# Kernel tuning notes

Measured on AMD Instinct MI355X. Metric: run time of the kernel, lower is better.

Reference implementation:

```python
import jax, jax.numpy as jnp
import numpy as np

B, T, C, D = 4, 2048, 48, 512
L = 16                    # transcript length per video (distinct labels)
K = 9                     # bdy_kernel
CS = 15                   # cs_kernel
N_TR = L - 1
N_CAND = 3 * N_TR         # candidate_mul * pt_num
WIN_LEN = int(T / L * 0.15)   # int(t / t_len * win_scale)
ALPHA, BETA, GAMMA, TEMP = 1.0, 1.0, 0.1, 0.1
LOG2 = float(np.log(2.0))

def _bdy_kernel():
    ker = np.zeros((K, K), np.float32)
    c = K // 2
    ker[:c, :c] = 1; ker[c:, c:] = 1
    ker[:c, c:] = -1; ker[c:, :c] = -1
    ker[c, c] = 0
    return jnp.asarray(ker)

BDY_KER = _bdy_kernel()

def bdy_score_fn(prob):
    # prob: [T, C]; sliding windows of size K over time (zero padded)
    c = K // 2
    pad = jnp.pad(prob, ((c, c), (0, 0)))
    win = pad[jnp.arange(T)[:, None] + jnp.arange(K)[None, :]]       # [T,K,C]
    p = win[:, :, None, :]                                           # [T,K,1,C]
    m = (p + win[:, None, :, :]) / 2                                 # [T,K,K,C]
    # torch F.kl_div((m+1e-32).log(), p) = p*(log p - log(m+1e-32)), xlogy(0)=0
    kl = jnp.sum(jnp.where(p > 0, p * (jnp.log(jnp.where(p > 0, p, 1.0)) - jnp.log(m + 1e-32)), 0.0), -1)
    js = (kl + jnp.swapaxes(kl, 1, 2)) / 2
    js = -(js / LOG2 * 2 - 1)                                        # [T,K,K]
    return jnp.mean(BDY_KER[None] * js, axis=(-1, -2))               # [T]

def dp(cls_score):
    # cls_score: [N_TR, N_CAND]; min-cost alignment DP, inner jj-loop vectorized
    cost = -cls_score
    n_tr, n_x = N_TR, N_CAND
    W = 2 * n_tr + 1
    col = jnp.arange(W)
    inf = jnp.float32(jnp.inf)
    tr_at = jnp.clip(col // 2, 0, n_tr - 1)
    even = (col % 2 == 0)
    ge2 = col >= 2

    def init_cols(ii):
        c0 = jnp.where(ii < n_x - n_tr, 0.0, inf)
        c1 = jnp.where(ii <= n_x - n_tr, cost[0, ii], inf)
        d1 = jnp.where(ii <= n_x - n_tr, 1, 0).astype(jnp.int32)
        return c0, c1, d1

    c0, c1, d1 = init_cols(0)
    row0 = jnp.full((W,), inf).at[0].set(c0).at[1].set(c1)
    dir0 = jnp.zeros((W,), jnp.int32).at[1].set(d1)

    def step(prev, ii):
        dm1 = jnp.concatenate([jnp.full((1,), inf), prev[:-1]])
        dm2 = jnp.concatenate([jnp.full((2,), inf), prev[:-2]])
        c_at = cost[:, ii][tr_at]
        even_val = jnp.minimum(prev, dm1)
        even_dir = jnp.where(prev < dm1, 0, 1).astype(jnp.int32)
        odd_val = c_at + jnp.minimum(dm1, dm2)
        odd_dir = jnp.where(dm1 < dm2, 1, 2).astype(jnp.int32)
        c0, c1, d1 = init_cols(ii)
        new = jnp.where(ge2, jnp.where(even, even_val, odd_val), inf)
        new = new.at[0].set(c0).at[1].set(c1)
        dirs = jnp.where(ge2, jnp.where(even, even_dir, odd_dir), 0).astype(jnp.int32)
        dirs = dirs.at[1].set(d1)
        return new, dirs

    last, dirs = jax.lax.scan(step, row0, jnp.arange(1, n_x))
    dir_mat = jnp.concatenate([dir0[None], dirs], 0)                 # [n_x, W]
    cur_j0 = jnp.where(last[2 * n_tr] < last[2 * n_tr - 1], 2 * n_tr, 2 * n_tr - 1).astype(jnp.int32)

    def bt(cur_j, x):
        ii, dir_row = x
        is_odd = (cur_j % 2) == 1
        out_idx = jnp.where(is_odd, cur_j // 2, jnp.int32(n_tr))     # n_tr = OOB -> dropped
        new_j = cur_j - dir_row[cur_j]
        return new_j, (out_idx, ii.astype(jnp.int32))

    _, (oi, ovals) = jax.lax.scan(bt, cur_j0, (jnp.arange(n_x), dir_mat), reverse=True)
    return jnp.zeros((n_tr,), jnp.int32).at[oi].set(ovals, mode='drop')

def detect(logit, tr):
    # logit: [T,C] (detached), tr: [L] ints -> boundary frame indices [N_TR]
    prob = jax.nn.softmax(logit, -1)
    score = bdy_score_fn(prob).at[0].set(-jnp.inf)
    backup = score
    pos = jnp.arange(T)

    def pick(s, _):
        i = jnp.argmax(s)
        return jnp.where(jnp.abs(pos - i) <= WIN_LEN, -jnp.inf, s), i

    _, cand = jax.lax.scan(pick, score, None, length=N_CAND)
    cand = jnp.sort(cand)                                            # [N_CAND]
    # class-transition score at candidate points
    cc = CS // 2
    pairs = jnp.pad(prob[:, tr], ((cc, cc), (0, 0)))                 # [T+2cc, L]
    win = pairs[cand[:, None] + jnp.arange(CS)[None, :]]             # [N_CAND, CS, L]
    first, second = win[:, :, :-1], win[:, :, 1:]
    k0 = jnp.where(jnp.arange(CS) < cc, 1.0, -1.0)[None, :, None]
    cls = jnp.sum(k0 * (first - second), axis=1) / (2 * CS)          # [N_CAND, N_TR]
    cls = cls.T + backup[cand][None, :]                              # [N_TR, N_CAND]
    return cand[dp(cls)]

def _forward(tok_logit, fr_logit, vid_multi_hot, feat, mask, transcript):
    y = vid_multi_hot
    tok_loss = jnp.mean(-(y * jax.nn.log_sigmoid(tok_logit) + (1 - y) * jax.nn.log_sigmoid(-tok_logit)))
    # boundary detection on detached logits
    bdy = jax.vmap(detect)(jax.lax.stop_gradient(fr_logit), transcript)   # [B, N_TR]
    pse = jax.vmap(lambda b, tr: tr[jnp.sum(jnp.arange(T)[:, None] >= b[None, :], axis=1)])(bdy, transcript)
    # frame CE (bgw==1.0 path, full mask so no -100 labels)
    logp = jax.nn.log_softmax(fr_logit, -1)
    ce = -jnp.take_along_axis(logp, pse[..., None], axis=-1)[..., 0]
    m = mask.astype(ce.dtype)
    fr_loss = jnp.sum(ce * m) / jnp.sum(m)
    # global-local contrast
    tok_feat = jax.lax.stop_gradient(feat[:, :C, :])
    fr_feat = feat[:, C:, :]

    def glc_one(tok, fr, pse_i, tr, m_i):
        labels = jnp.sort(tr)                                        # = unique(pse[mask]), distinct labels
        oh = (pse_i[None, :] == labels[:, None]).astype(fr.dtype) * m_i[None, :]
        cnt = jnp.maximum(jnp.sum(oh, 1, keepdims=True), 1.0)
        la = (oh @ fr) / cnt
        la = la / jnp.maximum(jnp.linalg.norm(la, axis=-1, keepdims=True), 1e-12)
        tk = tok / jnp.maximum(jnp.linalg.norm(tok, axis=-1, keepdims=True), 1e-12)
        sim = (la @ tk.T) / TEMP                                     # [L, C]
        return jnp.mean(-jnp.take_along_axis(jax.nn.log_softmax(sim, -1), labels[:, None], axis=-1))

    glc_loss = jnp.mean(jax.vmap(glc_one)(tok_feat, fr_feat, pse, transcript, mask.astype(feat.dtype)))
    return ALPHA * tok_loss + BETA * fr_loss + GAMMA * glc_loss

def setup_inputs() -> dict:
    key = jax.random.key(0)
    ks = jax.random.split(key, 5)
    tok_logit = jax.random.normal(ks[0], (B, C), jnp.float32)
    fr_logit = jax.random.normal(ks[1], (B, T, C), jnp.float32)
    mask = jnp.ones((B, T), bool)
    transcript = jax.vmap(lambda k: jax.random.permutation(k, C)[:L])(jax.random.split(ks[2], B)).astype(jnp.int32)
    vid_multi_hot = jax.random.uniform(ks[3], (B, C), jnp.float32)
    feat = jax.random.normal(ks[4], (B, C + T, D), jnp.float32)
    return {"epoch": 5, "tok_logit": tok_logit, "fr_logit": fr_logit, "mask": mask,
            "transcript": transcript, "vid_multi_hot": vid_multi_hot, "feat": feat}

def reference(epoch, tok_logit, fr_logit, mask, transcript, vid_multi_hot, feat):
    # epoch >= warm_epc (=0), so the full loss path runs
    return _forward(tok_logit, fr_logit, vid_multi_hot, feat, mask, transcript)
```

## Files before the change

### kernel.cpp

```cpp
#include <hip/hip_runtime.h>
#include <math.h>

#define BB 4
#define TT 2048
#define CC 48
#define DD 512
#define LL 16
#define NTR 15
#define NCAND 45
#define WINLEN 19
#define CSW 15
#define CCHALF 7

static __device__ __forceinline__ float wave_reduce_sum(float v) {
    for (int off = 32; off; off >>= 1) v += __shfl_down(v, off);
    return v;
}

#define DPPMAX(x, ctrl) fmaxf((x), __int_as_float(__builtin_amdgcn_update_dpp( \
    __float_as_int(x), __float_as_int(x), (ctrl), 0xF, 0xF, false)))

__global__ __launch_bounds__(256) void k_lse(const float* __restrict__ fr,
                                             float* __restrict__ lse) {
    int row = blockIdx.x * 4 + (threadIdx.x >> 6);
    int lane = threadIdx.x & 63;
    float xv = (lane < CC) ? fr[(size_t)row * CC + lane] : -INFINITY;
    float m = xv;
    for (int off = 32; off; off >>= 1) m = fmaxf(m, __shfl_down(m, off));
    m = __shfl(m, 0);
    float e = (lane < CC) ? __expf(xv - m) : 0.f;
    float s = wave_reduce_sum(e);
    if (lane == 0) lse[row] = m + __logf(s);
}

__global__ __launch_bounds__(256) void k_score(const float* __restrict__ fr,
                                               const float* __restrict__ lse,
                                               float* __restrict__ score) {
    int t_base = (blockIdx.x * 4) % TT;
    int b = (blockIdx.x * 4) / TT;
    __shared__ float sp[12][CC];
    __shared__ float slp[12][CC];
    __shared__ float lse_s[12];
    int tid = threadIdx.x;
    int wave = tid >> 6, lane = tid & 63;
    if (tid < 12) {
        int r = t_base - 4 + tid;
        lse_s[tid] = (r >= 0 && r < TT) ? lse[b * TT + r] : 0.f;
    }
    __syncthreads();
    for (int idx = tid; idx < 12 * CC; idx += 256) {
        int i = idx / CC, c = idx - (idx / CC) * CC;
        int r = t_base - 4 + i;
        float pv = 0.f, lv = 0.f;
        if (r >= 0 && r < TT) {
            float x = fr[((size_t)b * TT + r) * CC + c];
            lv = x - lse_s[i];
            pv = __expf(lv);
        }
        sp[i][c] = pv;
        slp[i][c] = lv;
    }
    __syncthreads();
    int t = t_base + wave;
    float acc = 0.f;
    for (int idx = lane; idx < 4 * CC; idx += 64) {
        int i = idx / CC, c = idx - (idx / CC) * CC;
        acc += -2.f * sp[wave + i][c] * slp[wave + i][c];
    }
    for (int item = lane; item < 36 * CC; item += 64) {
        int pidx = item / CC, c = item - pidx * CC;
        int i = 0, rem = pidx;
        while (rem >= 8 - i) { rem -= 8 - i; ++i; }
        int j = i + 1 + rem;
        float wgt = ((i < 4) == (j < 4)) ? 1.f : -1.f;
        float pi = sp[wave + i][c], pj = sp[wave + j][c];
        float logm = __logf(0.5f * (pi + pj) + 1e-32f);
        acc -= wgt * (pi + pj) * logm;
    }
    acc = wave_reduce_sum(acc);
    if (lane == 0) {
        const float SC = -2.0f / (81.0f * 0.6931471805599453f);
        score[(size_t)b * TT + t] = (t == 0) ? -INFINITY : SC * acc;
    }
}

__global__ __launch_bounds__(64) void k_pick(const float* __restrict__ score,
                                             int* __restrict__ cand,
                                             float* __restrict__ backup) {
    int b = blockIdx.x;
    int lane = threadIdx.x;
    __shared__ float s[64 * 33];
    __shared__ int cl[NCAND];
    for (int t = lane; t < TT; t += 64) s[t + (t >> 5)] = score[(size_t)b * TT + t];
    __syncthreads();
    float v[32];
    #pragma unroll
    for (int k = 0; k < 32; ++k) v[k] = s[lane * 33 + k];
    int base = lane << 5;
    for (int it = 0; it < NCAND; ++it) {
        float best = -INFINITY; int bi = 0;
        #pragma unroll
        for (int k = 31; k >= 0; --k)
            if (v[k] >= best) { best = v[k]; bi = k; }
        float m = best;
        m = DPPMAX(m, 0x111); m = DPPMAX(m, 0x112);
        m = DPPMAX(m, 0x114); m = DPPMAX(m, 0x118);
        m = DPPMAX(m, 0x142); m = DPPMAX(m, 0x143);
        float gmax = __int_as_float(__builtin_amdgcn_readlane(__float_as_int(m), 63));
        unsigned long long ball = __ballot(best == gmax);
        int sl = (int)(__ffsll((long long)ball) - 1);
        int mp = __builtin_amdgcn_readlane(base + bi, sl);
        if (lane == 0) cl[it] = mp;
        int llo = mp - WINLEN - base;
        int lhi = mp + WINLEN - base;
        unsigned lowm = (llo <= 0) ? 0xffffffffu : ((llo >= 32) ? 0u : ~((1u << llo) - 1u));
        unsigned him  = (lhi >= 31) ? 0xffffffffu : ((lhi < 0) ? 0u : ((2u << lhi) - 1u));
        unsigned wm = lowm & him;
        #pragma unroll
        for (int k = 0; k < 32; ++k)
            if (wm & (1u << k)) v[k] = -INFINITY;
    }
    __syncthreads();
    if (lane < NCAND) {
        int my = cl[lane];
        int rank = 0;
        for (int i = 0; i < NCAND; ++i) rank += (cl[i] < my) ? 1 : 0;
        cand[b * 64 + rank] = my;
        backup[b * 64 + rank] = s[my + (my >> 5)];
    }
}

__global__ __launch_bounds__(256) void k_cls(const float* __restrict__ fr,
                                             const float* __restrict__ lse,
                                             const int* __restrict__ cand,
                                             const float* __restrict__ backup,
                                             const int* __restrict__ transcript,
                                             float* __restrict__ cost_g) {
    int ii = blockIdx.x, b = blockIdx.y;
    __shared__ float win[CSW][LL + 1];
    __shared__ int tr_s[LL];
    int tid = threadIdx.x;
    if (tid < LL) tr_s[tid] = transcript[b * LL + tid];
    __syncthreads();
    int cpos = cand[b * 64 + ii];
    if (tid < CSW * LL) {
        int k = tid >> 4, m2 = tid & 15;
        int r = cpos - CCHALF + k;
        float p = 0.f;
        if (r >= 0 && r < TT) {
            size_t ro = (size_t)b * TT + r;
            p = __expf(fr[ro * CC + tr_s[m2]] - lse[ro]);
        }
        win[k][m2] = p;
    }
    __syncthreads();
    if (tid < NTR) {
        int j = tid;
        float sum = 0.f;
        #pragma unroll
        for (int k = 0; k < CSW; ++k)
            sum += ((k < CCHALF) ? 1.f : -1.f) * (win[k][j] - win[k][j + 1]);
        cost_g[(b * NTR + j) * NCAND + ii] = -(sum / 30.f + backup[b * 64 + ii]);
    }
}

__global__ __launch_bounds__(256) void k_dp(const float* __restrict__ fr,
                                            const float* __restrict__ lse,
                                            const int* __restrict__ cand,
                                            const float* __restrict__ cost_g,
                                            const int* __restrict__ transcript,
                                            int* __restrict__ labels_out,
                                            int* __restrict__ rowmap,
                                            float* __restrict__ fr_part,
                                            float* __restrict__ la) {
    int b = blockIdx.x;
    __shared__ float cost[NTR][NCAND];
    __shared__ int tr_s[LL];
    __shared__ int cand_s[NCAND];
    __shared__ signed char dir_mat[NCAND][32];
    __shared__ int bdy_s[NTR];
    __shared__ int rank_s[LL];
    __shared__ float redf[4];
    int tid = threadIdx.x;
    int wave = tid >> 6, lane = tid & 63;
    if (tid < LL) tr_s[tid] = transcript[b * LL + tid];
    if (tid < NCAND) cand_s[tid] = cand[b * 64 + tid];

    {
        float4 z = {0.f, 0.f, 0.f, 0.f};
        float4* lz = (float4*)(la + (size_t)b * LL * DD);
        #pragma unroll
        for (int i = 0; i < LL * DD / 4 / 256; ++i) lz[i * 256 + tid] = z;
    }
    for (int e = tid; e < NTR * NCAND; e += 256) {
        int j = e / NCAND, ii = e - j * NCAND;
        cost[j][ii] = cost_g[b * NTR * NCAND + e];
    }
    __syncthreads();

    if (tid < 64) {
        float prev = INFINITY;
        if (tid == 0) prev = 0.f;
        if (tid == 1) prev = cost[0][0];
        if (tid < 31) dir_mat[0][tid] = (tid == 1) ? (signed char)1 : (signed char)0;
        for (int ii = 1; ii < NCAND; ++ii) {
            float dm1 = __shfl_up(prev, 1); if (tid < 1) dm1 = INFINITY;
            float dm2 = __shfl_up(prev, 2); if (tid < 2) dm2 = INFINITY;
            int trat = tid >> 1; if (trat > NTR - 1) trat = NTR - 1;
            float c_at = cost[trat][ii];
            float ev = fminf(prev, dm1);
            int ed = (prev < dm1) ? 0 : 1;
            float ov = c_at + fminf(dm1, dm2);
            int od = (dm1 < dm2) ? 1 : 2;
            float nv; int nd;
            if (tid >= 2) {
                if ((tid & 1) == 0) { nv = ev; nd = ed; }
                else { nv = ov; nd = od; }
            } else { nv = INFINITY; nd = 0; }
            if (tid == 0) { nv = (ii < NCAND - NTR) ? 0.f : INFINITY; nd = 0; }
            if (tid == 1) {
                nv = (ii <= NCAND - NTR) ? cost[0][ii] : INFINITY;
                nd = (ii <= NCAND - NTR) ? 1 : 0;
            }
            prev = nv;
            if (tid < 31) dir_mat[ii][tid] = (signed char)nd;
        }
        float v29 = __shfl(prev, 29);
        float v30 = __shfl(prev, 30);
        if (tid == 0) {
            int cur = (v30 < v29) ? 30 : 29;
            for (int ii = NCAND - 1; ii >= 0; --ii) {
                if (cur & 1) bdy_s[cur >> 1] = cand_s[ii];
                cur -= (int)dir_mat[ii][cur];
            }
        }
    }
    __syncthreads();

    if (tid < LL) {
        int myv = tr_s[tid];
        int r2 = 0;
        #pragma unroll
        for (int l2 = 0; l2 < LL; ++l2) r2 += (tr_s[l2] < myv) ? 1 : 0;
        rank_s[tid] = r2;
        labels_out[b * LL + r2] = myv;
    }
    __syncthreads();

    float facc = 0.f;
    for (int t = tid; t < TT; t += 256) {
        int cnt = 0;
        #pragma unroll
        for (int j = 0; j < NTR; ++j) cnt += (t >= bdy_s[j]) ? 1 : 0;
        int pv = tr_s[cnt];
        rowmap[b * TT + t] = rank_s[cnt];
        size_t ro = (size_t)b * TT + t;
        facc += lse[ro] - fr[ro * CC + pv];
    }
    facc = wave_reduce_sum(facc);
    if (lane == 0) redf[wave] = facc;
    __syncthreads();
    if (tid == 0) fr_part[b] = redf[0] + redf[1] + redf[2] + redf[3];
}

__global__ __launch_bounds__(256) void k_la(const float* __restrict__ feat,
                                            const int* __restrict__ rowmap,
                                            float* __restrict__ la) {
    int b = blockIdx.y;
    int t0 = blockIdx.x * 32;
    int tid = threadIdx.x;
    const float* frf = feat + ((size_t)b * (CC + TT) + CC) * DD;
    __shared__ int rm[32];
    if (tid < 32) rm[tid] = rowmap[b * TT + t0 + tid];
    __syncthreads();
    float ax = 0.f, ay = 0.f;
    int cur = rm[0];
    for (int k = 0; k < 32; ++k) {
        int r = rm[k];
        if (r != cur) {
            float* dst = la + ((size_t)b * LL + cur) * DD + tid * 2;
            atomicAdd(dst, ax);
            atomicAdd(dst + 1, ay);
            ax = 0.f; ay = 0.f; cur = r;
        }
        const float2* p = (const float2*)(frf + (size_t)(t0 + k) * DD);
        float2 v = p[tid];
        ax += v.x; ay += v.y;
    }
    float* dst = la + ((size_t)b * LL + cur) * DD + tid * 2;
    atomicAdd(dst, ax);
    atomicAdd(dst + 1, ay);
}

__global__ __launch_bounds__(256) void k_glc(const float* __restrict__ feat,
                                             const float* __restrict__ la,
                                             float* __restrict__ dots,
                                             float* __restrict__ ntk) {
    int c = blockIdx.x, b = blockIdx.y;
    __shared__ float tok_s[DD];
    __shared__ float redv[4];
    int tid = threadIdx.x;
    int wave = tid >> 6, lane = tid & 63;
    const float* tr = feat + ((size_t)b * (CC + TT) + c) * DD;
    float2 tv = ((const float2*)tr)[tid];
    ((float2*)tok_s)[tid] = tv;
    float vv = tv.x * tv.x + tv.y * tv.y;
    vv = wave_reduce_sum(vv);
    if (lane == 0) redv[wave] = vv;
    __syncthreads();
    if (tid == 0)
        ntk[b * CC + c] = fmaxf(sqrtf(redv[0] + redv[1] + redv[2] + redv[3]), 1e-12f);
    for (int l = wave; l < LL; l += 4) {
        const float4* lar = (const float4*)(la + ((size_t)b * LL + l) * DD);
        const float4* ts = (const float4*)tok_s;
        float dot = 0.f;
        #pragma unroll
        for (int jj = 0; jj < 2; ++jj) {
            int j = lane + jj * 64;
            float4 a = lar[j]; float4 w = ts[j];
            dot += a.x * w.x + a.y * w.y + a.z * w.z + a.w * w.w;
        }
        dot = wave_reduce_sum(dot);
        if (lane == 0) dots[((size_t)b * LL + l) * CC + c] = dot;
    }
}

__global__ __launch_bounds__(64) void k_term(const float* __restrict__ la,
                                             const float* __restrict__ dots,
                                             const float* __restrict__ ntk,
                                             const int* __restrict__ labels,
                                             float* __restrict__ terms) {
    int l = blockIdx.x, b = blockIdx.y;
    int lane = threadIdx.x;
    const float4* lar = (const float4*)(la + ((size_t)b * LL + l) * DD);
    float ss = 0.f;
    #pragma unroll
    for (int jj = 0; jj < 2; ++jj) {
        float4 a = lar[lane + jj * 64];
        ss += a.x * a.x + a.y * a.y + a.z * a.z + a.w * a.w;
    }
    ss = wave_reduce_sum(ss);
    float nla = fmaxf(sqrtf(__shfl(ss, 0)), 1e-12f);
    float sim = -INFINITY;
    if (lane < CC)
        sim = dots[((size_t)b * LL + l) * CC + lane] * 10.0f / (nla * ntk[b * CC + lane]);
    float mx = sim;
    for (int off = 32; off; off >>= 1) mx = fmaxf(mx, __shfl_down(mx, off));
    mx = __shfl(mx, 0);
    float e = (lane < CC) ? expf(sim - mx) : 0.f;
    float se = wave_reduce_sum(e);
    se = __shfl(se, 0);
    int lab = labels[b * LL + l];
    float sim_lab = __shfl(sim, lab);
    if (lane == 0) terms[b * LL + l] = (mx + logf(se)) - sim_lab;
}

__global__ __launch_bounds__(256) void k_combine(const float* __restrict__ tok_logit,
                                                 const float* __restrict__ vid,
                                                 const float* __restrict__ fr_part,
                                                 const float* __restrict__ terms,
                                                 float* __restrict__ out) {
    int tid = threadIdx.x;
    __shared__ float red[4];
    __shared__ float gterm;
    float acc = 0.f;
    if (tid < BB * CC) {
        float x = tok_logit[tid], y = vid[tid];
        float lsp = fminf(x, 0.f) - log1pf(expf(-fabsf(x)));
        float lsn = fminf(-x, 0.f) - log1pf(expf(-fabsf(x)));
        acc = -(y * lsp + (1.f - y) * lsn);
    }
    float w = wave_reduce_sum(acc);
    if ((tid & 63) == 0) red[tid >> 6] = w;
    if (tid < 64) {
        float g = terms[tid];
        g = wave_reduce_sum(g);
        if (tid == 0) gterm = g;
    }
    __syncthreads();
    if (tid == 0) {
        float s_tok = (red[0] + red[1] + red[2] + red[3]) / (float)(BB * CC);
        float sfr = fr_part[0] + fr_part[1] + fr_part[2] + fr_part[3];
        float s_fr = sfr / (float)(BB * TT);
        float glc = gterm / (float)(BB * LL);
        out[0] = s_tok + s_fr + 0.1f * glc;
    }
}

extern "C" void kernel_launch(void* const* d_in, const int* in_sizes, int n_in,
                              void* d_out, int out_size, void* d_ws, size_t ws_size,
                              hipStream_t stream) {
    (void)in_sizes; (void)n_in; (void)out_size; (void)ws_size;
    const float* tok_logit  = (const float*)d_in[1];
    const float* fr_logit   = (const float*)d_in[2];
    const int*   transcript = (const int*)d_in[4];
    const float* vid        = (const float*)d_in[5];
    const float* feat       = (const float*)d_in[6];

    char* ws = (char*)d_ws;
    float* lse     = (float*)(ws + 0);
    float* score   = (float*)(ws + 32768);
    float* la      = (float*)(ws + 65536);
    float* dots    = (float*)(ws + 196608);
    float* ntk     = (float*)(ws + 208896);
    float* terms   = (float*)(ws + 209664);
    float* fr_part = (float*)(ws + 209920);
    int*   labels  = (int*)(ws + 210176);
    int*   rowmap  = (int*)(ws + 210432);
    int*   cand    = (int*)(ws + 243200);
    float* backup  = (float*)(ws + 244224);
    float* cost_g  = (float*)(ws + 245248);
    float* out     = (float*)d_out;

    k_lse<<<BB * TT / 4, 256, 0, stream>>>(fr_logit, lse);
    k_score<<<BB * TT / 4, 256, 0, stream>>>(fr_logit, lse, score);
    k_pick<<<BB, 64, 0, stream>>>(score, cand, backup);
    k_cls<<<dim3(NCAND, BB), 256, 0, stream>>>(fr_logit, lse, cand, backup,
                                               transcript, cost_g);
    k_dp<<<BB, 256, 0, stream>>>(fr_logit, lse, cand, cost_g, transcript,
                                 labels, rowmap, fr_part, la);
    k_la<<<dim3(TT / 32, BB), 256, 0, stream>>>(feat, rowmap, la);
    k_glc<<<dim3(CC, BB), 256, 0, stream>>>(feat, la, dots, ntk);
    k_term<<<dim3(LL, BB), 64, 0, stream>>>(la, dots, ntk, labels, terms);
    k_combine<<<1, 256, 0, stream>>>(tok_logit, vid, fr_part, terms, out);
}
```

Before: 166.4 us.

## Fuse log-sum-exp into score kernel and merge glc with term kernel

The separate k_lse pass is removed. k_score now computes the row log-sum-exp for its 12-row halo tile in shared memory and writes the center rows' lse for the later kernels. The k_glc and k_term kernels are merged into one kernel per (label, batch) that computes the dot products, norms and softmax term directly. This drops two launches and the dots/ntk round trips, at the cost of recomputing lse for halo rows and re-reading token features once per label.

```diff
diff --git a/kernel.cpp b/kernel.cpp
--- a/kernel.cpp
+++ b/kernel.cpp
@@ -20,21 +20,8 @@
 #define DPPMAX(x, ctrl) fmaxf((x), __int_as_float(__builtin_amdgcn_update_dpp( \
     __float_as_int(x), __float_as_int(x), (ctrl), 0xF, 0xF, false)))
 
-__global__ __launch_bounds__(256) void k_lse(const float* __restrict__ fr,
-                                             float* __restrict__ lse) {
-    int row = blockIdx.x * 4 + (threadIdx.x >> 6);
-    int lane = threadIdx.x & 63;
-    float xv = (lane < CC) ? fr[(size_t)row * CC + lane] : -INFINITY;
-    float m = xv;
-    for (int off = 32; off; off >>= 1) m = fmaxf(m, __shfl_down(m, off));
-    m = __shfl(m, 0);
-    float e = (lane < CC) ? __expf(xv - m) : 0.f;
-    float s = wave_reduce_sum(e);
-    if (lane == 0) lse[row] = m + __logf(s);
-}
-
 __global__ __launch_bounds__(256) void k_score(const float* __restrict__ fr,
-                                               const float* __restrict__ lse,
+                                               float* __restrict__ lse,
                                                float* __restrict__ score) {
     int t_base = (blockIdx.x * 4) % TT;
     int b = (blockIdx.x * 4) / TT;
@@ -43,25 +30,36 @@
     __shared__ float lse_s[12];
     int tid = threadIdx.x;
     int wave = tid >> 6, lane = tid & 63;
-    if (tid < 12) {
-        int r = t_base - 4 + tid;
-        lse_s[tid] = (r >= 0 && r < TT) ? lse[b * TT + r] : 0.f;
-    }
-    __syncthreads();
     for (int idx = tid; idx < 12 * CC; idx += 256) {
         int i = idx / CC, c = idx - (idx / CC) * CC;
         int r = t_base - 4 + i;
-        float pv = 0.f, lv = 0.f;
-        if (r >= 0 && r < TT) {
-            float x = fr[((size_t)b * TT + r) * CC + c];
-            lv = x - lse_s[i];
-            pv = __expf(lv);
-        }
+        sp[i][c] = (r >= 0 && r < TT) ? fr[((size_t)b * TT + r) * CC + c] : 0.f;
+    }
+    __syncthreads();
+    for (int q = 0; q < 3; ++q) {
+        int i = wave * 3 + q;
+        int r = t_base - 4 + i;
+        bool valid = (r >= 0 && r < TT);
+        float xv = (lane < CC && valid) ? sp[i][lane] : -INFINITY;
+        float m = xv;
+        for (int off = 32; off; off >>= 1) m = fmaxf(m, __shfl_down(m, off));
+        m = __shfl(m, 0);
+        float e = (lane < CC && valid) ? __expf(xv - m) : 0.f;
+        float s = wave_reduce_sum(e);
+        if (lane == 0) lse_s[i] = valid ? (m + __logf(s)) : 0.f;
+    }
+    __syncthreads();
+    for (int idx = tid; idx < 12 * CC; idx += 256) {
+        int i = idx / CC, c = idx - (idx / CC) * CC;
+        int r = t_base - 4 + i;
+        float lv = 0.f, pv = 0.f;
+        if (r >= 0 && r < TT) { lv = sp[i][c] - lse_s[i]; pv = __expf(lv); }
+        slp[i][c] = lv;
         sp[i][c] = pv;
-        slp[i][c] = lv;
     }
     __syncthreads();
     int t = t_base + wave;
+    if (lane == 0) lse[(size_t)b * TT + t] = lse_s[wave + 4];
     float acc = 0.f;
     for (int idx = lane; idx < 4 * CC; idx += 64) {
         int i = idx / CC, c = idx - (idx / CC) * CC;
@@ -292,67 +290,54 @@
     atomicAdd(dst + 1, ay);
 }
 
-__global__ __launch_bounds__(256) void k_glc(const float* __restrict__ feat,
-                                             const float* __restrict__ la,
-                                             float* __restrict__ dots,
-                                             float* __restrict__ ntk) {
-    int c = blockIdx.x, b = blockIdx.y;
-    __shared__ float tok_s[DD];
+__global__ __launch_bounds__(256) void k_glcterm(const float* __restrict__ feat,
+                                                 const float* __restrict__ la,
+                                                 const int* __restrict__ labels,
+                                                 float* __restrict__ terms) {
+    int l = blockIdx.x, b = blockIdx.y;
+    __shared__ float la_s[DD];
+    __shared__ float sim_s[CC];
     __shared__ float redv[4];
     int tid = threadIdx.x;
     int wave = tid >> 6, lane = tid & 63;
-    const float* tr = feat + ((size_t)b * (CC + TT) + c) * DD;
-    float2 tv = ((const float2*)tr)[tid];
-    ((float2*)tok_s)[tid] = tv;
-    float vv = tv.x * tv.x + tv.y * tv.y;
-    vv = wave_reduce_sum(vv);
-    if (lane == 0) redv[wave] = vv;
-    __syncthreads();
-    if (tid == 0)
-        ntk[b * CC + c] = fmaxf(sqrtf(redv[0] + redv[1] + redv[2] + redv[3]), 1e-12f);
-    for (int l = wave; l < LL; l += 4) {
-        const float4* lar = (const float4*)(la + ((size_t)b * LL + l) * DD);
-        const float4* ts = (const float4*)tok_s;
-        float dot = 0.f;
+    const float* lar = la + ((size_t)b * LL + l) * DD;
+    float2 lv = ((const float2*)lar)[tid];
+    ((float2*)la_s)[tid] = lv;
+    float ss = lv.x * lv.x + lv.y * lv.y;
+    ss = wave_reduce_sum(ss);
+    if (lane == 0) redv[wave] = ss;
+    __syncthreads();
+    float nla = fmaxf(sqrtf(redv[0] + redv[1] + redv[2] + redv[3]), 1e-12f);
+    float inv_nla = 10.0f / nla;
+    for (int c = wave; c < CC; c += 4) {
+        const float4* tr = (const float4*)(feat + ((size_t)b * (CC + TT) + c) * DD);
+        const float4* ls = (const float4*)la_s;
+        float dot = 0.f, vv = 0.f;
         #pragma unroll
         for (int jj = 0; jj < 2; ++jj) {
             int j = lane + jj * 64;
-            float4 a = lar[j]; float4 w = ts[j];
+            float4 a = ls[j]; float4 w = tr[j];
             dot += a.x * w.x + a.y * w.y + a.z * w.z + a.w * w.w;
+            vv  += w.x * w.x + w.y * w.y + w.z * w.z + w.w * w.w;
         }
         dot = wave_reduce_sum(dot);
-        if (lane == 0) dots[((size_t)b * LL + l) * CC + c] = dot;
-    }
-}
-
-__global__ __launch_bounds__(64) void k_term(const float* __restrict__ la,
-                                             const float* __restrict__ dots,
-                                             const float* __restrict__ ntk,
-                                             const int* __restrict__ labels,
-                                             float* __restrict__ terms) {
-    int l = blockIdx.x, b = blockIdx.y;
-    int lane = threadIdx.x;
-    const float4* lar = (const float4*)(la + ((size_t)b * LL + l) * DD);
-    float ss = 0.f;
-    #pragma unroll
-    for (int jj = 0; jj < 2; ++jj) {
-        float4 a = lar[lane + jj * 64];
-        ss += a.x * a.x + a.y * a.y + a.z * a.z + a.w * a.w;
-    }
-    ss = wave_reduce_sum(ss);
-    float nla = fmaxf(sqrtf(__shfl(ss, 0)), 1e-12f);
-    float sim = -INFINITY;
-    if (lane < CC)
-        sim = dots[((size_t)b * LL + l) * CC + lane] * 10.0f / (nla * ntk[b * CC + lane]);
-    float mx = sim;
-    for (int off = 32; off; off >>= 1) mx = fmaxf(mx, __shfl_down(mx, off));
-    mx = __shfl(mx, 0);
-    float e = (lane < CC) ? expf(sim - mx) : 0.f;
-    float se = wave_reduce_sum(e);
-    se = __shfl(se, 0);
-    int lab = labels[b * LL + l];
-    float sim_lab = __shfl(sim, lab);
-    if (lane == 0) terms[b * LL + l] = (mx + logf(se)) - sim_lab;
+        vv  = wave_reduce_sum(vv);
+        if (lane == 0)
+            sim_s[c] = dot * inv_nla / fmaxf(sqrtf(vv), 1e-12f);
+    }
+    __syncthreads();
+    if (tid < 64) {
+        float sim = (lane < CC) ? sim_s[lane] : -INFINITY;
+        float mx = sim;
+        for (int off = 32; off; off >>= 1) mx = fmaxf(mx, __shfl_down(mx, off));
+        mx = __shfl(mx, 0);
+        float e = (lane < CC) ? expf(sim - mx) : 0.f;
+        float se = wave_reduce_sum(e);
+        se = __shfl(se, 0);
+        int lab = labels[b * LL + l];
+        float sim_lab = __shfl(sim, lab);
+        if (lane == 0) terms[b * LL + l] = (mx + logf(se)) - sim_lab;
+    }
 }
 
 __global__ __launch_bounds__(256) void k_combine(const float* __restrict__ tok_logit,
@@ -401,8 +386,6 @@
     float* lse     = (float*)(ws + 0);
     float* score   = (float*)(ws + 32768);
     float* la      = (float*)(ws + 65536);
-    float* dots    = (float*)(ws + 196608);
-    float* ntk     = (float*)(ws + 208896);
     float* terms   = (float*)(ws + 209664);
     float* fr_part = (float*)(ws + 209920);
     int*   labels  = (int*)(ws + 210176);
@@ -412,7 +395,6 @@
     float* cost_g  = (float*)(ws + 245248);
     float* out     = (float*)d_out;
 
-    k_lse<<<BB * TT / 4, 256, 0, stream>>>(fr_logit, lse);
     k_score<<<BB * TT / 4, 256, 0, stream>>>(fr_logit, lse, score);
     k_pick<<<BB, 64, 0, stream>>>(score, cand, backup);
     k_cls<<<dim3(NCAND, BB), 256, 0, stream>>>(fr_logit, lse, cand, backup,
@@ -420,7 +402,6 @@
     k_dp<<<BB, 256, 0, stream>>>(fr_logit, lse, cand, cost_g, transcript,
                                  labels, rowmap, fr_part, la);
     k_la<<<dim3(TT / 32, BB), 256, 0, stream>>>(feat, rowmap, la);
-    k_glc<<<dim3(CC, BB), 256, 0, stream>>>(feat, la, dots, ntk);
-    k_term<<<dim3(LL, BB), 64, 0, stream>>>(la, dots, ntk, labels, terms);
+    k_glcterm<<<dim3(LL, BB), 256, 0, stream>>>(feat, la, labels, terms);
     k_combine<<<1, 256, 0, stream>>>(tok_logit, vid, fr_part, terms, out);
 }
```

New measurement: 169.7 us. 1.02x slower.
